# Performance work log

Measured on AMD Instinct MI355X. Metric: run time of the kernel, lower is better.

Reference implementation:

```python
import jax, jax.numpy as jnp
import numpy as np
import math

N_HEADS = 16
D_KV = 64
D_MODEL = 1024
NUM_BUCKETS = 32
MAX_DISTANCE = 128


def _relative_position_bucket(rel_pos):
    # encoder (is_decoder=False): bidirectional buckets
    num_buckets = NUM_BUCKETS // 2  # 16
    rel_buckets = (rel_pos > 0).astype(jnp.int32) * num_buckets
    rel_pos = jnp.abs(rel_pos)
    max_exact = num_buckets // 2  # 8
    is_small = rel_pos < max_exact
    rel_pos_large = max_exact + (
        jnp.log(rel_pos.astype(jnp.float32) / max_exact)
        / math.log(MAX_DISTANCE / max_exact)
        * (num_buckets - max_exact)
    ).astype(jnp.int32)
    rel_pos_large = jnp.minimum(rel_pos_large, num_buckets - 1)
    return rel_buckets + jnp.where(is_small, rel_pos, rel_pos_large)


def setup_inputs() -> dict:
    key = jax.random.key(0)
    ks = jax.random.split(key, 6)
    s = 1.0 / math.sqrt(D_MODEL)
    return {
        "hidden_states": jax.random.normal(ks[0], (2, 2048, D_MODEL), jnp.float32),
        "Wq": jax.random.normal(ks[1], (D_MODEL, N_HEADS * D_KV), jnp.float32) * s,
        "Wk": jax.random.normal(ks[2], (D_MODEL, N_HEADS * D_KV), jnp.float32) * s,
        "Wv": jax.random.normal(ks[3], (D_MODEL, N_HEADS * D_KV), jnp.float32) * s,
        "Wo": jax.random.normal(ks[4], (N_HEADS * D_KV, D_MODEL), jnp.float32) * s,
        "rel_bias": jax.random.normal(ks[5], (NUM_BUCKETS, N_HEADS), jnp.float32),
    }


def reference(hidden_states, Wq, Wk, Wv, Wo, rel_bias):
    b, seq, _ = hidden_states.shape
    q = (hidden_states @ Wq).reshape(b, seq, N_HEADS, D_KV)
    k = (hidden_states @ Wk).reshape(b, seq, N_HEADS, D_KV)
    v = (hidden_states @ Wv).reshape(b, seq, N_HEADS, D_KV)

    # relative position bias: [1, n_heads, q_len, k_len]
    ctx = jnp.arange(seq, dtype=jnp.int32)[:, None]
    mem = jnp.arange(seq, dtype=jnp.int32)[None, :]
    buckets = _relative_position_bucket(mem - ctx)  # [q, k]
    pos_bias = rel_bias[buckets]                    # [q, k, h]
    pos_bias = jnp.transpose(pos_bias, (2, 0, 1))[None]  # [1, h, q, k]

    # NOTE: T5-style attention has no 1/sqrt(d) scaling
    attn = jnp.einsum('binc,bjnc->bnij', q, k) + pos_bias
    attn = jax.nn.softmax(attn.astype(jnp.float32), axis=-1).astype(attn.dtype)
    o = jnp.einsum('bnij,bjnc->binc', attn, v).reshape(b, seq, N_HEADS * D_KV)
    return o @ Wo
```

## Files before the change

### kernel.cpp

```cpp
#include <hip/hip_runtime.h>
#include <hip/hip_bf16.h>
#include <math.h>

#define DM   1024
#define HD   1024
#define NH   16
#define DK   64
#define SEQ  2048
#define BATCH 2

#define LOG2E 1.4426950408889634f
#define FIXB 32.0f

typedef __attribute__((ext_vector_type(8))) short bf16x8;
typedef __attribute__((ext_vector_type(4))) float f32x4;

static __device__ __forceinline__ short f2b(float f) {
  union { float f; unsigned u; } v; v.f = f;
  unsigned r = (v.u + 0x7fffu + ((v.u >> 16) & 1u)) >> 16;
  return (short)r;
}

static __device__ __forceinline__ int cvt_pk(float lo, float hi) {
  int r;
  asm("v_cvt_pk_bf16_f32 %0, %1, %2" : "=v"(r) : "v"(lo), "v"(hi));
  return r;
}

static __device__ __forceinline__ void gload_lds16(const void* g, void* l) {
  __builtin_amdgcn_global_load_lds(
      (const __attribute__((address_space(1))) void*)g,
      (__attribute__((address_space(3))) void*)l, 16, 0, 0);
}


__global__ __launch_bounds__(256) void k_cvt_h(const float* __restrict__ in,
                                               short* __restrict__ out) {
  int i = (blockIdx.x * 256 + threadIdx.x) * 8;
  float4 a = *reinterpret_cast<const float4*>(in + i);
  float4 b = *reinterpret_cast<const float4*>(in + i + 4);
  bf16x8 o;
  o[0] = f2b(a.x); o[1] = f2b(a.y); o[2] = f2b(a.z); o[3] = f2b(a.w);
  o[4] = f2b(b.x); o[5] = f2b(b.y); o[6] = f2b(b.z); o[7] = f2b(b.w);
  *reinterpret_cast<bf16x8*>(out + i) = o;
}

__global__ __launch_bounds__(256) void k_wtrans(const float* __restrict__ Wq,
                                                const float* __restrict__ Wk,
                                                const float* __restrict__ Wv,
                                                const float* __restrict__ Wo,
                                                short* __restrict__ Wts) {
  const float* src = (blockIdx.z == 0) ? Wq : (blockIdx.z == 1) ? Wk
                   : (blockIdx.z == 2) ? Wv : Wo;
  const float scl = (blockIdx.z == 0) ? LOG2E : 1.0f;
  short* dst = Wts + (size_t)blockIdx.z * DM * HD;
  __shared__ float t[32][33];
  int tx = threadIdx.x & 31, ty = threadIdx.x >> 5;
  int k0 = blockIdx.y * 32, n0 = blockIdx.x * 32;
#pragma unroll
  for (int i = 0; i < 4; ++i)
    t[ty + i * 8][tx] = src[(size_t)(k0 + ty + i * 8) * 1024 + n0 + tx];
  __syncthreads();
#pragma unroll
  for (int i = 0; i < 4; ++i)
    dst[(size_t)(n0 + ty + i * 8) * 1024 + k0 + tx] = f2b(t[tx][ty + i * 8] * scl);
}

__global__ __launch_bounds__(256) void k_bias(const float* __restrict__ rel_bias,
                                              float* __restrict__ btab) {
  int idx = blockIdx.x * 256 + threadIdx.x;
  int h = idx >> 12, pos = idx & 4095;
  int delta = pos - 2047;
  int rb = (delta > 0) ? 16 : 0;
  int ar = (delta < 0) ? -delta : delta;
  int bb;
  if (ar < 8) bb = ar;
  else {
    bb = 8 + (int)(logf((float)ar * 0.125f) * (8.0f / 2.7725887222397811f));
    if (bb > 15) bb = 15;
  }
  btab[idx] = rel_bias[(rb + bb) * NH + h] * LOG2E;
}

__global__ __launch_bounds__(256) void k_vtrans(const short* __restrict__ Vb,
                                                short* __restrict__ Vt) {
  int bh = blockIdx.y, b = bh >> 4, h = bh & 15;
  int st = blockIdx.x * 64;
  __shared__ short t[64][72];
  int tx = threadIdx.x & 15, ty = threadIdx.x >> 4;
#pragma unroll
  for (int i = 0; i < 4; ++i) {
    int row = ty + i * 16;
    *reinterpret_cast<short4*>(&t[row][tx * 4]) =
        *reinterpret_cast<const short4*>(
            &Vb[(size_t)(b * SEQ + st + row) * HD + h * 64 + tx * 4]);
  }
  __syncthreads();
  const int chunk = tx >> 3, bb = tx & 7;
  const int p = ((bb & 3) << 1) | (bb >> 2);
  const int kvpos = st + chunk * 32 + p * 4;
#pragma unroll
  for (int i = 0; i < 4; ++i) {
    int dk = ty + i * 16;
    short4 v = make_short4(t[tx * 4 + 0][dk], t[tx * 4 + 1][dk],
                           t[tx * 4 + 2][dk], t[tx * 4 + 3][dk]);
    *reinterpret_cast<short4*>(
        &Vt[(size_t)bh * DK * SEQ + (size_t)dk * SEQ + kvpos]) = v;
  }
}

template <int OUTF32>
__global__ __launch_bounds__(256) void k_gemm_bt(const short* __restrict__ A,
                                                 const short* __restrict__ Bt,
                                                 void* __restrict__ Cv,
                                                 size_t btz, size_t cz) {
  __shared__ __align__(16) short As[2][128 * 32];
  __shared__ __align__(16) short Bs[2][128 * 32];
  const int tid = threadIdx.x, w = tid >> 6, lane = tid & 63;
  const int wr = w >> 1, wc = w & 1, lg = lane >> 4, l15 = lane & 15;
  const int rowBase = blockIdx.y * 128, colBase = blockIdx.x * 128;
  const short* B = Bt + (size_t)blockIdx.z * btz;

  f32x4 acc[4][4];
#pragma unroll
  for (int m = 0; m < 4; ++m)
#pragma unroll
    for (int n = 0; n < 4; ++n) acc[m][n] = (f32x4){0.f, 0.f, 0.f, 0.f};

  const int c1 = w * 64 + lane, c2 = c1 + 256;
  const short* Ap1 = A + (size_t)(rowBase + (c1 >> 2)) * 1024 + (c1 & 3) * 8;
  const short* Ap2 = A + (size_t)(rowBase + (c2 >> 2)) * 1024 + (c2 & 3) * 8;
  const short* Bp1 = B + (size_t)(colBase + (c1 >> 2)) * 1024 + (c1 & 3) * 8;
  const short* Bp2 = B + (size_t)(colBase + (c2 >> 2)) * 1024 + (c2 & 3) * 8;

  {
    char* AsB = (char*)As[0];
    char* BsB = (char*)Bs[0];
    gload_lds16(Ap1, AsB + w * 1024);
    gload_lds16(Ap2, AsB + 4096 + w * 1024);
    gload_lds16(Bp1, BsB + w * 1024);
    gload_lds16(Bp2, BsB + 4096 + w * 1024);
  }
  asm volatile("s_waitcnt vmcnt(0)" ::: "memory");
  __syncthreads();
  int cur = 0;

  for (int k0 = 0; k0 < 1024; k0 += 32) {
    if (k0 + 32 < 1024) {
      char* AsB = (char*)As[cur ^ 1];
      char* BsB = (char*)Bs[cur ^ 1];
      gload_lds16(Ap1 + k0 + 32, AsB + w * 1024);
      gload_lds16(Ap2 + k0 + 32, AsB + 4096 + w * 1024);
      gload_lds16(Bp1 + k0 + 32, BsB + w * 1024);
      gload_lds16(Bp2 + k0 + 32, BsB + 4096 + w * 1024);
    }
    bf16x8 af[4], bfr[4];
#pragma unroll
    for (int m = 0; m < 4; ++m)
      af[m] = *reinterpret_cast<const bf16x8*>(
          &As[cur][(wr * 64 + m * 16 + l15) * 32 + lg * 8]);
#pragma unroll
    for (int n = 0; n < 4; ++n)
      bfr[n] = *reinterpret_cast<const bf16x8*>(
          &Bs[cur][(wc * 64 + n * 16 + l15) * 32 + lg * 8]);
#pragma unroll
    for (int m = 0; m < 4; ++m)
#pragma unroll
      for (int n = 0; n < 4; ++n)
        acc[m][n] =
            __builtin_amdgcn_mfma_f32_16x16x32_bf16(af[m], bfr[n], acc[m][n], 0, 0, 0);
    asm volatile("s_waitcnt vmcnt(0)" ::: "memory");
    __syncthreads();
    cur ^= 1;
  }

#pragma unroll
  for (int m = 0; m < 4; ++m)
#pragma unroll
    for (int n = 0; n < 4; ++n) {
      int col = colBase + wc * 64 + n * 16 + l15;
#pragma unroll
      for (int r = 0; r < 4; ++r) {
        int row = rowBase + wr * 64 + m * 16 + lg * 4 + r;
        if (OUTF32)
          ((float*)Cv)[(size_t)row * 1024 + col] = acc[m][n][r];
        else
          ((short*)Cv + (size_t)blockIdx.z * cz)[(size_t)row * 1024 + col] =
              f2b(acc[m][n][r]);
      }
    }
}

static __device__ __forceinline__ void stage_tile(const char* gbase, size_t grs,
                                                  char* lbase, int w, int lane) {
  const int r0 = w * 16 + (lane >> 3);
  const int cb = (lane & 7) * 16;
  const int sw = (r0 & 7) << 4;
  gload_lds16(gbase + (size_t)r0 * grs + (cb ^ sw), lbase + w * 2048);
  gload_lds16(gbase + (size_t)(r0 + 8) * grs + (cb ^ sw), lbase + w * 2048 + 1024);
}

__global__ __launch_bounds__(256, 4) void k_attn(const short* __restrict__ Qb,
                                                 const short* __restrict__ Kb,
                                                 const short* __restrict__ Vt,
                                                 const float* __restrict__ biasTab,
                                                 short* __restrict__ Ob) {
  const int j = blockIdx.x;
  const int orig = (j & 7) * 128 + (j >> 3);
  const int qt = orig & 31, bh = orig >> 5;
  const int b = bh >> 4, h = bh & 15;
  const int w = threadIdx.x >> 6, lane = threadIdx.x & 63;
  const int lg = lane >> 4, l15 = lane & 15;
  const int qbase = qt * 64 + w * 16;

  __shared__ __align__(16) char Ks[2][8192];
  __shared__ __align__(16) char Vs[2][8192];
  const int swz = (l15 & 7) << 4;

  const short* Qrow = Qb + (size_t)(b * SEQ + qbase + l15) * HD + h * 64 + lg * 8;
  bf16x8 q0 = *reinterpret_cast<const bf16x8*>(Qrow);
  bf16x8 q1 = *reinterpret_cast<const bf16x8*>(Qrow + 32);

  const char* Kg = (const char*)(Kb + (size_t)(b * SEQ) * HD + h * 64);
  const char* Vg = (const char*)(Vt + (size_t)bh * DK * SEQ);
  const float* btab = biasTab + h * 4096 + 2047;
  const float bias_hi = btab[1024];
  const float bias_lo = btab[-1024];

  f32x4 o[4];
#pragma unroll
  for (int c = 0; c < 4; ++c) o[c] = (f32x4){0.f, 0.f, 0.f, 0.f};
  float l_r = 0.f;

  const f32x4 z4 = (f32x4){0.f, 0.f, 0.f, 0.f};

  stage_tile(Kg, 2048, Ks[0], w, lane);
  stage_tile(Vg, 4096, Vs[0], w, lane);
  asm volatile("s_waitcnt vmcnt(0)" ::: "memory");
  __syncthreads();
  int cur = 0;

  for (int kt = 0; kt < 32; ++kt) {
    const int kvb = kt * 64;
    const int dkv = kvb - qbase;
    if (kt < 31) {
      stage_tile(Kg + (size_t)(kvb + 64) * 2048, 2048, Ks[cur ^ 1], w, lane);
      stage_tile(Vg + (size_t)(kvb + 64) * 2, 4096, Vs[cur ^ 1], w, lane);
    }
    const char* KsC = Ks[cur];
    f32x4 s[4];
    __builtin_amdgcn_s_setprio(1);
#pragma unroll
    for (int c = 0; c < 4; ++c) {
      const char* kr = KsC + (c * 16 + l15) * 128;
      bf16x8 kf0 = *reinterpret_cast<const bf16x8*>(kr + ((lg * 16) ^ swz));
      bf16x8 kf1 = *reinterpret_cast<const bf16x8*>(kr + ((64 + lg * 16) ^ swz));
      s[c] = __builtin_amdgcn_mfma_f32_16x16x32_bf16(kf0, q0, z4, 0, 0, 0);
      s[c] = __builtin_amdgcn_mfma_f32_16x16x32_bf16(kf1, q1, s[c], 0, 0, 0);
    }
    __builtin_amdgcn_s_setprio(0);
    float bu = 0.f;
    if (dkv >= 112) {
      bu = bias_hi;
    } else if (dkv <= -160) {
      bu = bias_lo;
    } else {
#pragma unroll
      for (int c = 0; c < 4; ++c)
#pragma unroll
        for (int r = 0; r < 4; ++r)
          s[c][r] += btab[dkv + c * 16 + lg * 4 + r - l15];
    }
    const float mb = FIXB - bu;
#pragma unroll
    for (int c = 0; c < 4; ++c)
#pragma unroll
      for (int r = 0; r < 4; ++r) s[c][r] = __builtin_exp2f(s[c][r] - mb);
    float r0 = (s[0][0] + s[0][1]) + (s[0][2] + s[0][3]);
    float r1 = (s[1][0] + s[1][1]) + (s[1][2] + s[1][3]);
    float r2 = (s[2][0] + s[2][1]) + (s[2][2] + s[2][3]);
    float r3 = (s[3][0] + s[3][1]) + (s[3][2] + s[3][3]);
    l_r += (r0 + r1) + (r2 + r3);
    int4 p0i, p1i;
    p0i.x = cvt_pk(s[0][0], s[0][1]); p0i.y = cvt_pk(s[0][2], s[0][3]);
    p0i.z = cvt_pk(s[1][0], s[1][1]); p0i.w = cvt_pk(s[1][2], s[1][3]);
    p1i.x = cvt_pk(s[2][0], s[2][1]); p1i.y = cvt_pk(s[2][2], s[2][3]);
    p1i.z = cvt_pk(s[3][0], s[3][1]); p1i.w = cvt_pk(s[3][2], s[3][3]);
    bf16x8 pb0 = *reinterpret_cast<bf16x8*>(&p0i);
    bf16x8 pb1 = *reinterpret_cast<bf16x8*>(&p1i);
    const char* VsC = Vs[cur];
    __builtin_amdgcn_s_setprio(1);
#pragma unroll
    for (int d = 0; d < 4; ++d) {
      const char* vr = VsC + (d * 16 + l15) * 128;
      bf16x8 v0f = *reinterpret_cast<const bf16x8*>(vr + ((lg * 16) ^ swz));
      bf16x8 v1f = *reinterpret_cast<const bf16x8*>(vr + ((64 + lg * 16) ^ swz));
      o[d] = __builtin_amdgcn_mfma_f32_16x16x32_bf16(v0f, pb0, o[d], 0, 0, 0);
      o[d] = __builtin_amdgcn_mfma_f32_16x16x32_bf16(v1f, pb1, o[d], 0, 0, 0);
    }
    __builtin_amdgcn_s_setprio(0);
    asm volatile("s_waitcnt vmcnt(0)" ::: "memory");
    __syncthreads();
    cur ^= 1;
  }
  l_r += __shfl_xor(l_r, 16, 64);
  l_r += __shfl_xor(l_r, 32, 64);
  float inv = 1.0f / l_r;
  const size_t orow = (size_t)(b * SEQ + qbase + l15) * HD + h * 64;
#pragma unroll
  for (int d = 0; d < 4; ++d) {
    int2 e;
    e.x = cvt_pk(o[d][0] * inv, o[d][1] * inv);
    e.y = cvt_pk(o[d][2] * inv, o[d][3] * inv);
    *reinterpret_cast<int2*>(&Ob[orow + d * 16 + lg * 4]) = e;
  }
}

extern "C" void kernel_launch(void* const* d_in, const int* in_sizes, int n_in,
                              void* d_out, int out_size, void* d_ws, size_t ws_size,
                              hipStream_t stream) {
  const float* H    = (const float*)d_in[0];
  const float* Wq   = (const float*)d_in[1];
  const float* Wk   = (const float*)d_in[2];
  const float* Wv   = (const float*)d_in[3];
  const float* Wo   = (const float*)d_in[4];
  const float* relb = (const float*)d_in[5];

  char* ws = (char*)d_ws;
  short* Hb   = (short*)(ws);
  short* Wts  = (short*)(ws + ((size_t)8 << 20));
  short* Qb   = (short*)(ws + ((size_t)16 << 20));
  short* Kb   = (short*)(ws + ((size_t)24 << 20));
  short* Vb   = (short*)(ws + ((size_t)32 << 20));
  short* Vt   = (short*)(ws + ((size_t)40 << 20));
  short* Ob   = (short*)(ws + ((size_t)48 << 20));
  float* btab = (float*)(ws + ((size_t)56 << 20));

  k_cvt_h<<<2048, 256, 0, stream>>>(H, Hb);
  k_wtrans<<<dim3(32, 32, 4), 256, 0, stream>>>(Wq, Wk, Wv, Wo, Wts);
  k_bias<<<256, 256, 0, stream>>>(relb, btab);

  k_gemm_bt<0><<<dim3(8, 32, 3), 256, 0, stream>>>(
      Hb, Wts, Qb, (size_t)1024 * 1024, (size_t)4096 * 1024);

  k_vtrans<<<dim3(32, 32), 256, 0, stream>>>(Vb, Vt);
  k_attn<<<1024, 256, 0, stream>>>(Qb, Kb, Vt, btab, Ob);

  k_gemm_bt<1><<<dim3(8, 32, 1), 256, 0, stream>>>(
      Ob, Wts + (size_t)3 * 1024 * 1024, d_out, 0, 0);
}
```

Before: 214.1 us.

## Triple-buffer LDS staging in GEMM and attention kernels with partial vmcnt waits

```diff
diff --git a/kernel.cpp b/kernel.cpp
--- a/kernel.cpp
+++ b/kernel.cpp
@@ -109,13 +109,22 @@
   }
 }
 
+static __device__ __forceinline__ void gemm_stage(const short* Ap1, const short* Ap2,
+                                                  const short* Bp1, const short* Bp2,
+                                                  int k0, char* AsB, char* BsB, int w) {
+  gload_lds16(Ap1 + k0, AsB + w * 1024);
+  gload_lds16(Ap2 + k0, AsB + 4096 + w * 1024);
+  gload_lds16(Bp1 + k0, BsB + w * 1024);
+  gload_lds16(Bp2 + k0, BsB + 4096 + w * 1024);
+}
+
 template <int OUTF32>
 __global__ __launch_bounds__(256) void k_gemm_bt(const short* __restrict__ A,
                                                  const short* __restrict__ Bt,
                                                  void* __restrict__ Cv,
                                                  size_t btz, size_t cz) {
-  __shared__ __align__(16) short As[2][128 * 32];
-  __shared__ __align__(16) short Bs[2][128 * 32];
+  __shared__ __align__(16) short As[3][128 * 32];
+  __shared__ __align__(16) short Bs[3][128 * 32];
   const int tid = threadIdx.x, w = tid >> 6, lane = tid & 63;
   const int wr = w >> 1, wc = w & 1, lg = lane >> 4, l15 = lane & 15;
   const int rowBase = blockIdx.y * 128, colBase = blockIdx.x * 128;
@@ -133,27 +142,17 @@
   const short* Bp1 = B + (size_t)(colBase + (c1 >> 2)) * 1024 + (c1 & 3) * 8;
   const short* Bp2 = B + (size_t)(colBase + (c2 >> 2)) * 1024 + (c2 & 3) * 8;
 
-  {
-    char* AsB = (char*)As[0];
-    char* BsB = (char*)Bs[0];
-    gload_lds16(Ap1, AsB + w * 1024);
-    gload_lds16(Ap2, AsB + 4096 + w * 1024);
-    gload_lds16(Bp1, BsB + w * 1024);
-    gload_lds16(Bp2, BsB + 4096 + w * 1024);
-  }
-  asm volatile("s_waitcnt vmcnt(0)" ::: "memory");
-  __syncthreads();
+  gemm_stage(Ap1, Ap2, Bp1, Bp2, 0, (char*)As[0], (char*)Bs[0], w);
+  gemm_stage(Ap1, Ap2, Bp1, Bp2, 32, (char*)As[1], (char*)Bs[1], w);
+  asm volatile("s_waitcnt vmcnt(4)" ::: "memory");
+  __builtin_amdgcn_s_barrier();
+  __builtin_amdgcn_sched_barrier(0);
   int cur = 0;
 
   for (int k0 = 0; k0 < 1024; k0 += 32) {
-    if (k0 + 32 < 1024) {
-      char* AsB = (char*)As[cur ^ 1];
-      char* BsB = (char*)Bs[cur ^ 1];
-      gload_lds16(Ap1 + k0 + 32, AsB + w * 1024);
-      gload_lds16(Ap2 + k0 + 32, AsB + 4096 + w * 1024);
-      gload_lds16(Bp1 + k0 + 32, BsB + w * 1024);
-      gload_lds16(Bp2 + k0 + 32, BsB + 4096 + w * 1024);
-    }
+    int nx2 = cur + 2; if (nx2 >= 3) nx2 -= 3;
+    if (k0 < 960)
+      gemm_stage(Ap1, Ap2, Bp1, Bp2, k0 + 64, (char*)As[nx2], (char*)Bs[nx2], w);
     bf16x8 af[4], bfr[4];
 #pragma unroll
     for (int m = 0; m < 4; ++m)
@@ -169,9 +168,14 @@
       for (int n = 0; n < 4; ++n)
         acc[m][n] =
             __builtin_amdgcn_mfma_f32_16x16x32_bf16(af[m], bfr[n], acc[m][n], 0, 0, 0);
-    asm volatile("s_waitcnt vmcnt(0)" ::: "memory");
-    __syncthreads();
-    cur ^= 1;
+    if (k0 < 960) {
+      asm volatile("s_waitcnt vmcnt(4)" ::: "memory");
+    } else {
+      asm volatile("s_waitcnt vmcnt(0)" ::: "memory");
+    }
+    __builtin_amdgcn_s_barrier();
+    __builtin_amdgcn_sched_barrier(0);
+    cur = cur + 1; if (cur >= 3) cur = 0;
   }
 
 #pragma unroll
@@ -200,7 +204,7 @@
   gload_lds16(gbase + (size_t)(r0 + 8) * grs + (cb ^ sw), lbase + w * 2048 + 1024);
 }
 
-__global__ __launch_bounds__(256, 4) void k_attn(const short* __restrict__ Qb,
+__global__ __launch_bounds__(256, 3) void k_attn(const short* __restrict__ Qb,
                                                  const short* __restrict__ Kb,
                                                  const short* __restrict__ Vt,
                                                  const float* __restrict__ biasTab,
@@ -213,8 +217,8 @@
   const int lg = lane >> 4, l15 = lane & 15;
   const int qbase = qt * 64 + w * 16;
 
-  __shared__ __align__(16) char Ks[2][8192];
-  __shared__ __align__(16) char Vs[2][8192];
+  __shared__ __align__(16) char Ks[3][8192];
+  __shared__ __align__(16) char Vs[3][8192];
   const int swz = (l15 & 7) << 4;
 
   const short* Qrow = Qb + (size_t)(b * SEQ + qbase + l15) * HD + h * 64 + lg * 8;
@@ -236,16 +240,20 @@
 
   stage_tile(Kg, 2048, Ks[0], w, lane);
   stage_tile(Vg, 4096, Vs[0], w, lane);
-  asm volatile("s_waitcnt vmcnt(0)" ::: "memory");
-  __syncthreads();
+  stage_tile(Kg + (size_t)64 * 2048, 2048, Ks[1], w, lane);
+  stage_tile(Vg + (size_t)64 * 2, 4096, Vs[1], w, lane);
+  asm volatile("s_waitcnt vmcnt(4)" ::: "memory");
+  __builtin_amdgcn_s_barrier();
+  __builtin_amdgcn_sched_barrier(0);
   int cur = 0;
 
   for (int kt = 0; kt < 32; ++kt) {
     const int kvb = kt * 64;
     const int dkv = kvb - qbase;
-    if (kt < 31) {
-      stage_tile(Kg + (size_t)(kvb + 64) * 2048, 2048, Ks[cur ^ 1], w, lane);
-      stage_tile(Vg + (size_t)(kvb + 64) * 2, 4096, Vs[cur ^ 1], w, lane);
+    int nx2 = cur + 2; if (nx2 >= 3) nx2 -= 3;
+    if (kt < 30) {
+      stage_tile(Kg + (size_t)(kvb + 128) * 2048, 2048, Ks[nx2], w, lane);
+      stage_tile(Vg + (size_t)(kvb + 128) * 2, 4096, Vs[nx2], w, lane);
     }
     const char* KsC = Ks[cur];
     f32x4 s[4];
@@ -299,9 +307,14 @@
       o[d] = __builtin_amdgcn_mfma_f32_16x16x32_bf16(v1f, pb1, o[d], 0, 0, 0);
     }
     __builtin_amdgcn_s_setprio(0);
-    asm volatile("s_waitcnt vmcnt(0)" ::: "memory");
-    __syncthreads();
-    cur ^= 1;
+    if (kt < 30) {
+      asm volatile("s_waitcnt vmcnt(4)" ::: "memory");
+    } else {
+      asm volatile("s_waitcnt vmcnt(0)" ::: "memory");
+    }
+    __builtin_amdgcn_s_barrier();
+    __builtin_amdgcn_sched_barrier(0);
+    cur = cur + 1; if (cur >= 3) cur = 0;
   }
   l_r += __shfl_xor(l_r, 16, 64);
   l_r += __shfl_xor(l_r, 32, 64);
```

Result: slower. 227.1 us (+6.1%).

## Use 128-query attention blocks of 512 threads and narrow output GEMM tile

Applied to the files above, without the earlier changes.

```diff
diff --git a/kernel.cpp b/kernel.cpp
--- a/kernel.cpp
+++ b/kernel.cpp
@@ -109,23 +109,25 @@
   }
 }
 
-template <int OUTF32>
+template <int OUTF32, int TN>
 __global__ __launch_bounds__(256) void k_gemm_bt(const short* __restrict__ A,
                                                  const short* __restrict__ Bt,
                                                  void* __restrict__ Cv,
                                                  size_t btz, size_t cz) {
+  constexpr int NN = TN / 32;
+  constexpr int CW = TN / 2;
   __shared__ __align__(16) short As[2][128 * 32];
-  __shared__ __align__(16) short Bs[2][128 * 32];
+  __shared__ __align__(16) short Bs[2][TN * 32];
   const int tid = threadIdx.x, w = tid >> 6, lane = tid & 63;
   const int wr = w >> 1, wc = w & 1, lg = lane >> 4, l15 = lane & 15;
-  const int rowBase = blockIdx.y * 128, colBase = blockIdx.x * 128;
+  const int rowBase = blockIdx.y * 128, colBase = blockIdx.x * TN;
   const short* B = Bt + (size_t)blockIdx.z * btz;
 
-  f32x4 acc[4][4];
+  f32x4 acc[4][NN];
 #pragma unroll
   for (int m = 0; m < 4; ++m)
 #pragma unroll
-    for (int n = 0; n < 4; ++n) acc[m][n] = (f32x4){0.f, 0.f, 0.f, 0.f};
+    for (int n = 0; n < NN; ++n) acc[m][n] = (f32x4){0.f, 0.f, 0.f, 0.f};
 
   const int c1 = w * 64 + lane, c2 = c1 + 256;
   const short* Ap1 = A + (size_t)(rowBase + (c1 >> 2)) * 1024 + (c1 & 3) * 8;
@@ -139,46 +141,46 @@
     gload_lds16(Ap1, AsB + w * 1024);
     gload_lds16(Ap2, AsB + 4096 + w * 1024);
     gload_lds16(Bp1, BsB + w * 1024);
-    gload_lds16(Bp2, BsB + 4096 + w * 1024);
+    if (TN == 128) gload_lds16(Bp2, BsB + 4096 + w * 1024);
   }
   asm volatile("s_waitcnt vmcnt(0)" ::: "memory");
   __syncthreads();
-  int cur = 0;
-
+
+#pragma unroll 2
   for (int k0 = 0; k0 < 1024; k0 += 32) {
+    const int cu = (k0 >> 5) & 1;
     if (k0 + 32 < 1024) {
-      char* AsB = (char*)As[cur ^ 1];
-      char* BsB = (char*)Bs[cur ^ 1];
+      char* AsB = (char*)As[cu ^ 1];
+      char* BsB = (char*)Bs[cu ^ 1];
       gload_lds16(Ap1 + k0 + 32, AsB + w * 1024);
       gload_lds16(Ap2 + k0 + 32, AsB + 4096 + w * 1024);
       gload_lds16(Bp1 + k0 + 32, BsB + w * 1024);
-      gload_lds16(Bp2 + k0 + 32, BsB + 4096 + w * 1024);
-    }
-    bf16x8 af[4], bfr[4];
+      if (TN == 128) gload_lds16(Bp2 + k0 + 32, BsB + 4096 + w * 1024);
+    }
+    bf16x8 af[4], bfr[NN];
 #pragma unroll
     for (int m = 0; m < 4; ++m)
       af[m] = *reinterpret_cast<const bf16x8*>(
-          &As[cur][(wr * 64 + m * 16 + l15) * 32 + lg * 8]);
-#pragma unroll
-    for (int n = 0; n < 4; ++n)
+          &As[cu][(wr * 64 + m * 16 + l15) * 32 + lg * 8]);
+#pragma unroll
+    for (int n = 0; n < NN; ++n)
       bfr[n] = *reinterpret_cast<const bf16x8*>(
-          &Bs[cur][(wc * 64 + n * 16 + l15) * 32 + lg * 8]);
+          &Bs[cu][(wc * CW + n * 16 + l15) * 32 + lg * 8]);
 #pragma unroll
     for (int m = 0; m < 4; ++m)
 #pragma unroll
-      for (int n = 0; n < 4; ++n)
+      for (int n = 0; n < NN; ++n)
         acc[m][n] =
             __builtin_amdgcn_mfma_f32_16x16x32_bf16(af[m], bfr[n], acc[m][n], 0, 0, 0);
     asm volatile("s_waitcnt vmcnt(0)" ::: "memory");
     __syncthreads();
-    cur ^= 1;
   }
 
 #pragma unroll
   for (int m = 0; m < 4; ++m)
 #pragma unroll
-    for (int n = 0; n < 4; ++n) {
-      int col = colBase + wc * 64 + n * 16 + l15;
+    for (int n = 0; n < NN; ++n) {
+      int col = colBase + wc * CW + n * 16 + l15;
 #pragma unroll
       for (int r = 0; r < 4; ++r) {
         int row = rowBase + wr * 64 + m * 16 + lg * 4 + r;
@@ -191,27 +193,27 @@
     }
 }
 
-static __device__ __forceinline__ void stage_tile(const char* gbase, size_t grs,
-                                                  char* lbase, int w, int lane) {
-  const int r0 = w * 16 + (lane >> 3);
-  const int cb = (lane & 7) * 16;
+static __device__ __forceinline__ void stage_tile8(const char* gbase, size_t grs,
+                                                   char* lbase, int tid) {
+  const int r0 = tid >> 3;
+  const int cb = (tid & 7) * 16;
   const int sw = (r0 & 7) << 4;
-  gload_lds16(gbase + (size_t)r0 * grs + (cb ^ sw), lbase + w * 2048);
-  gload_lds16(gbase + (size_t)(r0 + 8) * grs + (cb ^ sw), lbase + w * 2048 + 1024);
-}
-
-__global__ __launch_bounds__(256, 4) void k_attn(const short* __restrict__ Qb,
+  gload_lds16(gbase + (size_t)r0 * grs + (cb ^ sw), lbase + (tid & ~63) * 16);
+}
+
+__global__ __launch_bounds__(512, 4) void k_attn(const short* __restrict__ Qb,
                                                  const short* __restrict__ Kb,
                                                  const short* __restrict__ Vt,
                                                  const float* __restrict__ biasTab,
                                                  short* __restrict__ Ob) {
   const int j = blockIdx.x;
-  const int orig = (j & 7) * 128 + (j >> 3);
-  const int qt = orig & 31, bh = orig >> 5;
+  const int orig = (j & 7) * 64 + (j >> 3);
+  const int qt = orig & 15, bh = orig >> 4;
   const int b = bh >> 4, h = bh & 15;
-  const int w = threadIdx.x >> 6, lane = threadIdx.x & 63;
+  const int tid = threadIdx.x;
+  const int w = tid >> 6, lane = tid & 63;
   const int lg = lane >> 4, l15 = lane & 15;
-  const int qbase = qt * 64 + w * 16;
+  const int qbase = qt * 128 + w * 16;
 
   __shared__ __align__(16) char Ks[2][8192];
   __shared__ __align__(16) char Vs[2][8192];
@@ -234,20 +236,21 @@
 
   const f32x4 z4 = (f32x4){0.f, 0.f, 0.f, 0.f};
 
-  stage_tile(Kg, 2048, Ks[0], w, lane);
-  stage_tile(Vg, 4096, Vs[0], w, lane);
+  stage_tile8(Kg, 2048, Ks[0], tid);
+  stage_tile8(Vg, 4096, Vs[0], tid);
   asm volatile("s_waitcnt vmcnt(0)" ::: "memory");
   __syncthreads();
-  int cur = 0;
-
+
+#pragma unroll 2
   for (int kt = 0; kt < 32; ++kt) {
+    const int cu = kt & 1;
     const int kvb = kt * 64;
     const int dkv = kvb - qbase;
     if (kt < 31) {
-      stage_tile(Kg + (size_t)(kvb + 64) * 2048, 2048, Ks[cur ^ 1], w, lane);
-      stage_tile(Vg + (size_t)(kvb + 64) * 2, 4096, Vs[cur ^ 1], w, lane);
-    }
-    const char* KsC = Ks[cur];
+      stage_tile8(Kg + (size_t)(kvb + 64) * 2048, 2048, Ks[cu ^ 1], tid);
+      stage_tile8(Vg + (size_t)(kvb + 64) * 2, 4096, Vs[cu ^ 1], tid);
+    }
+    const char* KsC = Ks[cu];
     f32x4 s[4];
     __builtin_amdgcn_s_setprio(1);
 #pragma unroll
@@ -288,7 +291,7 @@
     p1i.z = cvt_pk(s[3][0], s[3][1]); p1i.w = cvt_pk(s[3][2], s[3][3]);
     bf16x8 pb0 = *reinterpret_cast<bf16x8*>(&p0i);
     bf16x8 pb1 = *reinterpret_cast<bf16x8*>(&p1i);
-    const char* VsC = Vs[cur];
+    const char* VsC = Vs[cu];
     __builtin_amdgcn_s_setprio(1);
 #pragma unroll
     for (int d = 0; d < 4; ++d) {
@@ -301,7 +304,6 @@
     __builtin_amdgcn_s_setprio(0);
     asm volatile("s_waitcnt vmcnt(0)" ::: "memory");
     __syncthreads();
-    cur ^= 1;
   }
   l_r += __shfl_xor(l_r, 16, 64);
   l_r += __shfl_xor(l_r, 32, 64);
@@ -340,12 +342,12 @@
   k_wtrans<<<dim3(32, 32, 4), 256, 0, stream>>>(Wq, Wk, Wv, Wo, Wts);
   k_bias<<<256, 256, 0, stream>>>(relb, btab);
 
-  k_gemm_bt<0><<<dim3(8, 32, 3), 256, 0, stream>>>(
+  k_gemm_bt<0, 128><<<dim3(8, 32, 3), 256, 0, stream>>>(
       Hb, Wts, Qb, (size_t)1024 * 1024, (size_t)4096 * 1024);
 
   k_vtrans<<<dim3(32, 32), 256, 0, stream>>>(Vb, Vt);
-  k_attn<<<1024, 256, 0, stream>>>(Qb, Kb, Vt, btab, Ob);
-
-  k_gemm_bt<1><<<dim3(8, 32, 1), 256, 0, stream>>>(
+  k_attn<<<512, 512, 0, stream>>>(Qb, Kb, Vt, btab, Ob);
+
+  k_gemm_bt<1, 64><<<dim3(16, 32, 1), 256, 0, stream>>>(
       Ob, Wts + (size_t)3 * 1024 * 1024, d_out, 0, 0);
 }
```

Measured after the change: 205.7 us. 1.04x faster.
